# Optimization experiments

Measured on AMD Instinct MI355X. Metric: run time of the kernel, lower is better.

Reference implementation:

```python
import jax, jax.numpy as jnp
import numpy as np

S, B = 16384, 1
E = 2048          # encoder_hidden_size * num_enc_direction
H = 1024          # decoder_hidden_size
L = 2             # num_layer_dec
C = 5             # num_classes


def setup_inputs() -> dict:
    key = jax.random.key(0)
    ks = jax.random.split(key, 16)
    s = lambda fan_in: 1.0 / np.sqrt(fan_in)
    inp = {
        "encoder_hiddens": jax.random.normal(ks[0], (S, B, E), jnp.float32),
        "hidden": jax.random.normal(ks[1], (L, B, H), jnp.float32),
        "c": jax.random.normal(ks[2], (L, B, H), jnp.float32),
        # attn_alpha: Linear(2H + E, 1)
        "attn_w": jax.random.uniform(ks[3], (1, 2 * H + E), jnp.float32, -s(2 * H + E), s(2 * H + E)),
        "attn_b": jax.random.uniform(ks[4], (1,), jnp.float32, -s(2 * H + E), s(2 * H + E)),
        # LSTM layer 0: input E -> H
        "w_ih_l0": jax.random.uniform(ks[5], (4 * H, E), jnp.float32, -s(H), s(H)),
        "w_hh_l0": jax.random.uniform(ks[6], (4 * H, H), jnp.float32, -s(H), s(H)),
        "b_ih_l0": jax.random.uniform(ks[7], (4 * H,), jnp.float32, -s(H), s(H)),
        "b_hh_l0": jax.random.uniform(ks[8], (4 * H,), jnp.float32, -s(H), s(H)),
        # LSTM layer 1: input H -> H
        "w_ih_l1": jax.random.uniform(ks[9], (4 * H, H), jnp.float32, -s(H), s(H)),
        "w_hh_l1": jax.random.uniform(ks[10], (4 * H, H), jnp.float32, -s(H), s(H)),
        "b_ih_l1": jax.random.uniform(ks[11], (4 * H,), jnp.float32, -s(H), s(H)),
        "b_hh_l1": jax.random.uniform(ks[12], (4 * H,), jnp.float32, -s(H), s(H)),
        # fc: Linear(H, C)
        "fc_w": jax.random.uniform(ks[13], (C, H), jnp.float32, -s(H), s(H)),
        "fc_b": jax.random.uniform(ks[14], (C,), jnp.float32, -s(H), s(H)),
    }
    return inp


def _lstm_cell(x, h, c, w_ih, w_hh, b_ih, b_hh):
    # PyTorch gate order: i, f, g, o
    gates = x @ w_ih.T + b_ih + h @ w_hh.T + b_hh  # [B, 4H]
    i, f, g, o = jnp.split(gates, 4, axis=-1)
    c2 = jax.nn.sigmoid(f) * c + jax.nn.sigmoid(i) * jnp.tanh(g)
    h2 = jax.nn.sigmoid(o) * jnp.tanh(c2)
    return h2, c2


def reference(encoder_hiddens, hidden, c, attn_w, attn_b,
              w_ih_l0, w_hh_l0, b_ih_l0, b_hh_l0,
              w_ih_l1, w_hh_l1, b_ih_l1, b_hh_l1,
              fc_w, fc_b):
    h0, c0 = hidden[0], c[0]  # [B, H]
    # Vectorized per-timestep attn_alpha(concat(h0, c0, enc_i)):
    # split attn_w columns over [h0 | c0 | enc] and fuse the static part.
    w_h, w_c, w_e = attn_w[:, :H], attn_w[:, H:2 * H], attn_w[:, 2 * H:]
    static = h0 @ w_h.T + c0 @ w_c.T + attn_b            # [B, 1]
    scores = jnp.einsum('sbe,oe->sbo', encoder_hiddens, w_e) + static  # [S, B, 1]
    # Original applies softmax over dim=1 of a [B=1, 1] tensor per step -> all ones.
    attn = jax.nn.softmax(scores, axis=-1)               # [S, B, 1], identically 1.0
    # bmm(enc[B,E,S], attn[B,S,1]) == weighted sum over S
    attn_applied = jnp.einsum('sbe,sb->be', encoder_hiddens, attn[..., 0])  # [B, E]

    # 2-layer LSTM, single timestep
    h1, c1 = _lstm_cell(attn_applied, hidden[0], c[0], w_ih_l0, w_hh_l0, b_ih_l0, b_hh_l0)
    h2, c2 = _lstm_cell(h1, hidden[1], c[1], w_ih_l1, w_hh_l1, b_ih_l1, b_hh_l1)

    out = h2  # [B, H] == out.view(1*B, H)
    return out @ fc_w.T + fc_b  # [B, C]
```

## Files before the change

### kernel.cpp

```cpp
#include <hip/hip_runtime.h>
#include <hip/hip_bf16.h>
#include <math.h>

#define S_LEN 16384
#define E_DIM 2048
#define H_DIM 1024
#define G_DIM 4096
#define C_DIM 5

#define RCH 256
#define ROWS_PER_CHUNK (S_LEN / RCH)

#define WS_PART   0
#define WS_COLSUM (WS_PART + RCH * E_DIM)
#define WS_H1     (WS_COLSUM + E_DIM)
#define WS_H2     (WS_H1 + H_DIM)

__global__ __launch_bounds__(256) void colsum_partial_k(
    const float4* __restrict__ enc, float4* __restrict__ part) {
  const int E4 = E_DIM / 4;
  int colgroup = blockIdx.x & 1;
  int chunk = blockIdx.x >> 1;
  int e4 = colgroup * 256 + threadIdx.x;
  float4 acc = {0.f, 0.f, 0.f, 0.f};
  int r0 = chunk * ROWS_PER_CHUNK;
#pragma unroll 8
  for (int r = r0; r < r0 + ROWS_PER_CHUNK; ++r) {
    float4 v = enc[(size_t)r * E4 + e4];
    acc.x += v.x; acc.y += v.y; acc.z += v.z; acc.w += v.w;
  }
  part[chunk * E4 + e4] = acc;
}

__global__ __launch_bounds__(256) void colsum_final_k(
    const float* __restrict__ part, float* __restrict__ colsum) {
  int e = blockIdx.x * blockDim.x + threadIdx.x;
  float acc = 0.f;
#pragma unroll 8
  for (int ch = 0; ch < RCH; ++ch) acc += part[(size_t)ch * E_DIM + e];
  colsum[e] = acc;
}

__global__ __launch_bounds__(256) void lstm_fused_k(
    const float4* __restrict__ w_ih, const float4* __restrict__ w_hh,
    const float* __restrict__ b_ih, const float* __restrict__ b_hh,
    const float4* __restrict__ x, int xlen4,
    const float4* __restrict__ h, int hlen4,
    const float* __restrict__ c_prev,
    float* __restrict__ h_out) {
  __shared__ float smem[4];
  int wave = threadIdx.x >> 6;
  int lane = threadIdx.x & 63;
  int j = blockIdx.x;
  int row = wave * H_DIM + j;

  float acc = 0.f;
  const float4* wi = w_ih + (size_t)row * xlen4;
#pragma unroll
  for (int k = lane; k < xlen4; k += 64) {
    float4 w4 = wi[k];
    float4 v = x[k];
    acc += w4.x * v.x + w4.y * v.y + w4.z * v.z + w4.w * v.w;
  }
  const float4* wh = w_hh + (size_t)row * hlen4;
#pragma unroll
  for (int k = lane; k < hlen4; k += 64) {
    float4 w4 = wh[k];
    float4 v = h[k];
    acc += w4.x * v.x + w4.y * v.y + w4.z * v.z + w4.w * v.w;
  }
#pragma unroll
  for (int off = 32; off > 0; off >>= 1) acc += __shfl_down(acc, off);
  if (lane == 0) smem[wave] = acc + b_ih[row] + b_hh[row];
  __syncthreads();
  if (threadIdx.x == 0) {
    float ig = smem[0], fg = smem[1], gg = smem[2], og = smem[3];
    float si = 1.f / (1.f + expf(-ig));
    float sf = 1.f / (1.f + expf(-fg));
    float so = 1.f / (1.f + expf(-og));
    float c2 = sf * c_prev[j] + si * tanhf(gg);
    h_out[j] = so * tanhf(c2);
  }
}

__global__ __launch_bounds__(320) void fc_k(
    const float4* __restrict__ fc_w, const float* __restrict__ fc_b,
    const float4* __restrict__ h2, float* __restrict__ out) {
  int wave = threadIdx.x >> 6;
  int lane = threadIdx.x & 63;
  if (wave >= C_DIM) return;
  const int H4 = H_DIM / 4;
  float acc = 0.f;
  const float4* wr = fc_w + (size_t)wave * H4;
#pragma unroll
  for (int k = lane; k < H4; k += 64) {
    float4 w4 = wr[k];
    float4 v = h2[k];
    acc += w4.x * v.x + w4.y * v.y + w4.z * v.z + w4.w * v.w;
  }
#pragma unroll
  for (int off = 32; off > 0; off >>= 1) acc += __shfl_down(acc, off);
  if (lane == 0) out[wave] = acc + fc_b[wave];
}

extern "C" void kernel_launch(void* const* d_in, const int* in_sizes, int n_in,
                              void* d_out, int out_size, void* d_ws, size_t ws_size,
                              hipStream_t stream) {
  const float* enc     = (const float*)d_in[0];
  const float* hidden  = (const float*)d_in[1];
  const float* c_in    = (const float*)d_in[2];
  const float* w_ih_l0 = (const float*)d_in[5];
  const float* w_hh_l0 = (const float*)d_in[6];
  const float* b_ih_l0 = (const float*)d_in[7];
  const float* b_hh_l0 = (const float*)d_in[8];
  const float* w_ih_l1 = (const float*)d_in[9];
  const float* w_hh_l1 = (const float*)d_in[10];
  const float* b_ih_l1 = (const float*)d_in[11];
  const float* b_hh_l1 = (const float*)d_in[12];
  const float* fc_w    = (const float*)d_in[13];
  const float* fc_b    = (const float*)d_in[14];

  float* ws = (float*)d_ws;
  float* part   = ws + WS_PART;
  float* colsum = ws + WS_COLSUM;
  float* h1     = ws + WS_H1;
  float* h2     = ws + WS_H2;
  float* out    = (float*)d_out;

  colsum_partial_k<<<2 * RCH, 256, 0, stream>>>((const float4*)enc, (float4*)part);
  colsum_final_k<<<E_DIM / 256, 256, 0, stream>>>(part, colsum);

  lstm_fused_k<<<H_DIM, 256, 0, stream>>>(
      (const float4*)w_ih_l0, (const float4*)w_hh_l0, b_ih_l0, b_hh_l0,
      (const float4*)colsum, E_DIM / 4, (const float4*)hidden, H_DIM / 4,
      c_in, h1);

  lstm_fused_k<<<H_DIM, 256, 0, stream>>>(
      (const float4*)w_ih_l1, (const float4*)w_hh_l1, b_ih_l1, b_hh_l1,
      (const float4*)h1, H_DIM / 4, (const float4*)(hidden + H_DIM), H_DIM / 4,
      c_in + H_DIM, h2);

  fc_k<<<1, 320, 0, stream>>>((const float4*)fc_w, fc_b, (const float4*)h2, out);
}
```

Measured before the change: 62.03 us.

## Fuse decoder pipeline into one persistent kernel with grid-wide barriers

Replaces the five separate launches (two column-sum stages, two LSTM layers, fc) with a single 512-block kernel that moves between stages through atomic-counter grid barriers, after a memset that clears the barrier counters. The column sum now reduces rows within each block in shared memory first, so only 64 partial rows go to memory instead of 256. Each LSTM block now handles two hidden units, reusing the loaded x/h vectors across two weight rows. This aims to remove launch gaps and inter-kernel idle time, but relies on all 512 blocks being co-resident and adds spin-wait barrier overhead.

```diff
diff --git a/kernel.cpp b/kernel.cpp
--- a/kernel.cpp
+++ b/kernel.cpp
@@ -5,76 +5,91 @@
 #define S_LEN 16384
 #define E_DIM 2048
 #define H_DIM 1024
-#define G_DIM 4096
 #define C_DIM 5
 
-#define RCH 256
-#define ROWS_PER_CHUNK (S_LEN / RCH)
-
-#define WS_PART   0
-#define WS_COLSUM (WS_PART + RCH * E_DIM)
-#define WS_H1     (WS_COLSUM + E_DIM)
-#define WS_H2     (WS_H1 + H_DIM)
-
-__global__ __launch_bounds__(256) void colsum_partial_k(
-    const float4* __restrict__ enc, float4* __restrict__ part) {
-  const int E4 = E_DIM / 4;
-  int colgroup = blockIdx.x & 1;
-  int chunk = blockIdx.x >> 1;
-  int e4 = colgroup * 256 + threadIdx.x;
-  float4 acc = {0.f, 0.f, 0.f, 0.f};
-  int r0 = chunk * ROWS_PER_CHUNK;
-#pragma unroll 8
-  for (int r = r0; r < r0 + ROWS_PER_CHUNK; ++r) {
-    float4 v = enc[(size_t)r * E4 + e4];
-    acc.x += v.x; acc.y += v.y; acc.z += v.z; acc.w += v.w;
-  }
-  part[chunk * E4 + e4] = acc;
-}
-
-__global__ __launch_bounds__(256) void colsum_final_k(
-    const float* __restrict__ part, float* __restrict__ colsum) {
-  int e = blockIdx.x * blockDim.x + threadIdx.x;
-  float acc = 0.f;
-#pragma unroll 8
-  for (int ch = 0; ch < RCH; ++ch) acc += part[(size_t)ch * E_DIM + e];
-  colsum[e] = acc;
-}
-
-__global__ __launch_bounds__(256) void lstm_fused_k(
-    const float4* __restrict__ w_ih, const float4* __restrict__ w_hh,
-    const float* __restrict__ b_ih, const float* __restrict__ b_hh,
-    const float4* __restrict__ x, int xlen4,
-    const float4* __restrict__ h, int hlen4,
-    const float* __restrict__ c_prev,
-    float* __restrict__ h_out) {
-  __shared__ float smem[4];
-  int wave = threadIdx.x >> 6;
-  int lane = threadIdx.x & 63;
-  int j = blockIdx.x;
-  int row = wave * H_DIM + j;
-
-  float acc = 0.f;
-  const float4* wi = w_ih + (size_t)row * xlen4;
-#pragma unroll
-  for (int k = lane; k < xlen4; k += 64) {
-    float4 w4 = wi[k];
-    float4 v = x[k];
-    acc += w4.x * v.x + w4.y * v.y + w4.z * v.z + w4.w * v.w;
-  }
-  const float4* wh = w_hh + (size_t)row * hlen4;
-#pragma unroll
-  for (int k = lane; k < hlen4; k += 64) {
-    float4 w4 = wh[k];
-    float4 v = h[k];
-    acc += w4.x * v.x + w4.y * v.y + w4.z * v.z + w4.w * v.w;
-  }
-#pragma unroll
-  for (int off = 32; off > 0; off >>= 1) acc += __shfl_down(acc, off);
-  if (lane == 0) smem[wave] = acc + b_ih[row] + b_hh[row];
+#define NB 512
+#define NT 256
+
+#define NCTR 16
+#define BAR_BYTES (4 * NCTR * 16 * 4)
+
+__device__ __forceinline__ void gbar(int* bars, int k) {
   __syncthreads();
   if (threadIdx.x == 0) {
-    float ig = smem[0], fg = smem[1], gg = smem[2], og = smem[3];
+    __threadfence();
+    int* ctr = bars + (k * NCTR + (blockIdx.x & (NCTR - 1))) * 16;
+    __hip_atomic_fetch_add(ctr, 1, __ATOMIC_RELEASE, __HIP_MEMORY_SCOPE_AGENT);
+    int done = 0;
+    while (!done) {
+      int s = 0;
+#pragma unroll
+      for (int i = 0; i < NCTR; ++i)
+        s += __hip_atomic_load(bars + (k * NCTR + i) * 16, __ATOMIC_RELAXED,
+                               __HIP_MEMORY_SCOPE_AGENT);
+      done = (s == NB);
+      if (!done) __builtin_amdgcn_s_sleep(8);
+    }
+    __threadfence();
+  }
+  __syncthreads();
+}
+
+__device__ __forceinline__ float wave_sum(float v) {
+#pragma unroll
+  for (int off = 32; off > 0; off >>= 1) v += __shfl_down(v, off);
+  return v;
+}
+
+__device__ __forceinline__ float dot4(float4 a, float4 b) {
+  return a.x * b.x + a.y * b.y + a.z * b.z + a.w * b.w;
+}
+
+__device__ __forceinline__ void lstm_layer(
+    const float4* __restrict__ w_ih, int xlen4,
+    const float4* __restrict__ w_hh,
+    const float* __restrict__ b_ih, const float* __restrict__ b_hh,
+    const float4* __restrict__ x, const float4* __restrict__ h,
+    const float* __restrict__ c_prev, float* __restrict__ h_out,
+    float* smemf) {
+  int w = threadIdx.x >> 6;
+  int lane = threadIdx.x & 63;
+  int j0 = blockIdx.x * 2;
+  int rowA = w * H_DIM + j0;
+
+  float aA = 0.f, aB = 0.f;
+  const float4* wiA = w_ih + (size_t)rowA * xlen4;
+  const float4* wiB = wiA + xlen4;
+#pragma unroll 4
+  for (int k = lane; k < xlen4; k += 64) {
+    float4 xv = x[k];
+    float4 wa = wiA[k];
+    float4 wb = wiB[k];
+    aA += dot4(wa, xv);
+    aB += dot4(wb, xv);
+  }
+  const float4* whA = w_hh + (size_t)rowA * 256;
+  const float4* whB = whA + 256;
+#pragma unroll 4
+  for (int k = lane; k < 256; k += 64) {
+    float4 hv = h[k];
+    float4 wa = whA[k];
+    float4 wb = whB[k];
+    aA += dot4(wa, hv);
+    aB += dot4(wb, hv);
+  }
+  aA = wave_sum(aA);
+  aB = wave_sum(aB);
+  if (lane == 0) {
+    smemf[w * 2 + 0] = aA + b_ih[rowA] + b_hh[rowA];
+    smemf[w * 2 + 1] = aB + b_ih[rowA + 1] + b_hh[rowA + 1];
+  }
+  __syncthreads();
+  if (threadIdx.x < 2) {
+    int j = j0 + threadIdx.x;
+    float ig = smemf[0 + threadIdx.x];
+    float fg = smemf[2 + threadIdx.x];
+    float gg = smemf[4 + threadIdx.x];
+    float og = smemf[6 + threadIdx.x];
     float si = 1.f / (1.f + expf(-ig));
     float sf = 1.f / (1.f + expf(-fg));
     float so = 1.f / (1.f + expf(-og));
@@ -83,24 +98,83 @@
   }
 }
 
-__global__ __launch_bounds__(320) void fc_k(
-    const float4* __restrict__ fc_w, const float* __restrict__ fc_b,
-    const float4* __restrict__ h2, float* __restrict__ out) {
-  int wave = threadIdx.x >> 6;
-  int lane = threadIdx.x & 63;
-  if (wave >= C_DIM) return;
-  const int H4 = H_DIM / 4;
-  float acc = 0.f;
-  const float4* wr = fc_w + (size_t)wave * H4;
-#pragma unroll
-  for (int k = lane; k < H4; k += 64) {
-    float4 w4 = wr[k];
-    float4 v = h2[k];
-    acc += w4.x * v.x + w4.y * v.y + w4.z * v.z + w4.w * v.w;
-  }
-#pragma unroll
-  for (int off = 32; off > 0; off >>= 1) acc += __shfl_down(acc, off);
-  if (lane == 0) out[wave] = acc + fc_b[wave];
+__global__ __launch_bounds__(NT, 2) void decoder_mega_k(
+    const float* __restrict__ enc,
+    const float* __restrict__ hidden, const float* __restrict__ c_in,
+    const float* __restrict__ w_ih_l0, const float* __restrict__ w_hh_l0,
+    const float* __restrict__ b_ih_l0, const float* __restrict__ b_hh_l0,
+    const float* __restrict__ w_ih_l1, const float* __restrict__ w_hh_l1,
+    const float* __restrict__ b_ih_l1, const float* __restrict__ b_hh_l1,
+    const float* __restrict__ fc_w, const float* __restrict__ fc_b,
+    int* __restrict__ bars, float* __restrict__ part,
+    float* __restrict__ colsum, float* __restrict__ h1,
+    float* __restrict__ h2, float* __restrict__ out) {
+  __shared__ float4 smem4[NT];
+  float* smemf = (float*)smem4;
+
+  {
+    const float4* enc4 = (const float4*)enc;
+    int g = blockIdx.x >> 3;
+    int cb = blockIdx.x & 7;
+    int sub = threadIdx.x >> 6;
+    int lane = threadIdx.x & 63;
+    int c4 = cb * 64 + lane;
+    size_t base = ((size_t)(g * 256 + sub * 64)) * 512 + c4;
+    float4 acc = {0.f, 0.f, 0.f, 0.f};
+#pragma unroll 8
+    for (int r = 0; r < 64; ++r) {
+      float4 v = enc4[base + (size_t)r * 512];
+      acc.x += v.x; acc.y += v.y; acc.z += v.z; acc.w += v.w;
+    }
+    smem4[threadIdx.x] = acc;
+    __syncthreads();
+    if (threadIdx.x < 64) {
+      float4 a = smem4[threadIdx.x];
+      float4 b = smem4[64 + threadIdx.x];
+      float4 c = smem4[128 + threadIdx.x];
+      float4 d = smem4[192 + threadIdx.x];
+      float4 s;
+      s.x = (a.x + b.x) + (c.x + d.x);
+      s.y = (a.y + b.y) + (c.y + d.y);
+      s.z = (a.z + b.z) + (c.z + d.z);
+      s.w = (a.w + b.w) + (c.w + d.w);
+      ((float4*)part)[(size_t)g * 512 + cb * 64 + threadIdx.x] = s;
+    }
+  }
+  gbar(bars, 0);
+
+  if (blockIdx.x < 8) {
+    int col = blockIdx.x * NT + threadIdx.x;
+    float s = 0.f;
+#pragma unroll 8
+    for (int g = 0; g < 64; ++g) s += part[(size_t)g * E_DIM + col];
+    colsum[col] = s;
+  }
+  gbar(bars, 1);
+
+  lstm_layer((const float4*)w_ih_l0, E_DIM / 4, (const float4*)w_hh_l0,
+             b_ih_l0, b_hh_l0, (const float4*)colsum, (const float4*)hidden,
+             c_in, h1, smemf);
+  gbar(bars, 2);
+
+  lstm_layer((const float4*)w_ih_l1, H_DIM / 4, (const float4*)w_hh_l1,
+             b_ih_l1, b_hh_l1, (const float4*)h1,
+             (const float4*)(hidden + H_DIM), c_in + H_DIM, h2, smemf);
+  gbar(bars, 3);
+
+  if (blockIdx.x == 0) {
+    int w = threadIdx.x >> 6;
+    int lane = threadIdx.x & 63;
+    const float4* h24 = (const float4*)h2;
+    for (int r = w; r < C_DIM; r += 4) {
+      const float4* wr4 = (const float4*)fc_w + (size_t)r * 256;
+      float a = 0.f;
+#pragma unroll 4
+      for (int k = lane; k < 256; k += 64) a += dot4(wr4[k], h24[k]);
+      a = wave_sum(a);
+      if (lane == 0) out[r] = a + fc_b[r];
+    }
+  }
 }
 
 extern "C" void kernel_launch(void* const* d_in, const int* in_sizes, int n_in,
@@ -120,25 +194,18 @@
   const float* fc_w    = (const float*)d_in[13];
   const float* fc_b    = (const float*)d_in[14];
 
-  float* ws = (float*)d_ws;
-  float* part   = ws + WS_PART;
-  float* colsum = ws + WS_COLSUM;
-  float* h1     = ws + WS_H1;
-  float* h2     = ws + WS_H2;
+  int* bars = (int*)d_ws;
+  float* fws = (float*)((char*)d_ws + 4096);
+  float* part   = fws;
+  float* colsum = part + 64 * E_DIM;
+  float* h1     = colsum + E_DIM;
+  float* h2     = h1 + H_DIM;
   float* out    = (float*)d_out;
 
-  colsum_partial_k<<<2 * RCH, 256, 0, stream>>>((const float4*)enc, (float4*)part);
-  colsum_final_k<<<E_DIM / 256, 256, 0, stream>>>(part, colsum);
-
-  lstm_fused_k<<<H_DIM, 256, 0, stream>>>(
-      (const float4*)w_ih_l0, (const float4*)w_hh_l0, b_ih_l0, b_hh_l0,
-      (const float4*)colsum, E_DIM / 4, (const float4*)hidden, H_DIM / 4,
-      c_in, h1);
-
-  lstm_fused_k<<<H_DIM, 256, 0, stream>>>(
-      (const float4*)w_ih_l1, (const float4*)w_hh_l1, b_ih_l1, b_hh_l1,
-      (const float4*)h1, H_DIM / 4, (const float4*)(hidden + H_DIM), H_DIM / 4,
-      c_in + H_DIM, h2);
-
-  fc_k<<<1, 320, 0, stream>>>((const float4*)fc_w, fc_b, (const float4*)h2, out);
-}
+  hipMemsetAsync(d_ws, 0, BAR_BYTES, stream);
+
+  decoder_mega_k<<<NB, NT, 0, stream>>>(
+      enc, hidden, c_in, w_ih_l0, w_hh_l0, b_ih_l0, b_hh_l0,
+      w_ih_l1, w_hh_l1, b_ih_l1, b_hh_l1, fc_w, fc_b,
+      bars, part, colsum, h1, h2, out);
+}
```

After: 192.2 us. 210% more time.

## Restructure LSTM gate GEMVs to contiguous rows and fuse cell updates downstream

Applied to the files above, without the earlier changes.

The per-hidden-unit LSTM kernel is split into a gate-GEMV kernel whose blocks cover four consecutive gate rows, instead of one row from each gate block. The cell nonlinearity is moved into the next kernel: layer-0 cell math is recomputed redundantly by every block of the layer-1 gate kernel into shared memory, and layer-1 cell math is fused into the FC kernel. The column-sum reduction is split into twice as many chunks, and its final pass now has four waves share each column. The redundant per-block cell recomputation (1024 elements, four transcendentals each) adds compute to every block, and a single block now does all of the layer-1 cell math.

```diff
diff --git a/kernel.cpp b/kernel.cpp
--- a/kernel.cpp
+++ b/kernel.cpp
@@ -8,13 +8,25 @@
 #define G_DIM 4096
 #define C_DIM 5
 
-#define RCH 256
-#define ROWS_PER_CHUNK (S_LEN / RCH)
+#define CS_CHUNKS 512
+#define CS_ROWS   (S_LEN / CS_CHUNKS)
 
 #define WS_PART   0
-#define WS_COLSUM (WS_PART + RCH * E_DIM)
-#define WS_H1     (WS_COLSUM + E_DIM)
-#define WS_H2     (WS_H1 + H_DIM)
+#define WS_COLSUM (WS_PART + CS_CHUNKS * E_DIM)
+#define WS_G0     (WS_COLSUM + E_DIM)
+#define WS_G1     (WS_G0 + G_DIM)
+
+__device__ __forceinline__ float wave_sum(float v) {
+#pragma unroll
+  for (int off = 32; off > 0; off >>= 1) v += __shfl_down(v, off);
+  return v;
+}
+
+__device__ __forceinline__ float dot4(float4 a, float4 b) {
+  return a.x * b.x + a.y * b.y + a.z * b.z + a.w * b.w;
+}
+
+__device__ __forceinline__ float sigm(float x) { return 1.f / (1.f + expf(-x)); }
 
 __global__ __launch_bounds__(256) void colsum_partial_k(
     const float4* __restrict__ enc, float4* __restrict__ part) {
@@ -23,84 +35,113 @@
   int chunk = blockIdx.x >> 1;
   int e4 = colgroup * 256 + threadIdx.x;
   float4 acc = {0.f, 0.f, 0.f, 0.f};
-  int r0 = chunk * ROWS_PER_CHUNK;
+  size_t base = (size_t)chunk * CS_ROWS * E4 + e4;
 #pragma unroll 8
-  for (int r = r0; r < r0 + ROWS_PER_CHUNK; ++r) {
-    float4 v = enc[(size_t)r * E4 + e4];
+  for (int r = 0; r < CS_ROWS; ++r) {
+    float4 v = enc[base + (size_t)r * E4];
     acc.x += v.x; acc.y += v.y; acc.z += v.z; acc.w += v.w;
   }
-  part[chunk * E4 + e4] = acc;
+  part[(size_t)chunk * E4 + e4] = acc;
 }
 
 __global__ __launch_bounds__(256) void colsum_final_k(
     const float* __restrict__ part, float* __restrict__ colsum) {
-  int e = blockIdx.x * blockDim.x + threadIdx.x;
+  __shared__ float red[4][64];
+  int lane = threadIdx.x & 63;
+  int grp = threadIdx.x >> 6;
+  int col = blockIdx.x * 64 + lane;
   float acc = 0.f;
+  int c0 = grp * (CS_CHUNKS / 4);
 #pragma unroll 8
-  for (int ch = 0; ch < RCH; ++ch) acc += part[(size_t)ch * E_DIM + e];
-  colsum[e] = acc;
-}
-
-__global__ __launch_bounds__(256) void lstm_fused_k(
-    const float4* __restrict__ w_ih, const float4* __restrict__ w_hh,
-    const float* __restrict__ b_ih, const float* __restrict__ b_hh,
-    const float4* __restrict__ x, int xlen4,
-    const float4* __restrict__ h, int hlen4,
-    const float* __restrict__ c_prev,
-    float* __restrict__ h_out) {
-  __shared__ float smem[4];
-  int wave = threadIdx.x >> 6;
-  int lane = threadIdx.x & 63;
-  int j = blockIdx.x;
-  int row = wave * H_DIM + j;
-
-  float acc = 0.f;
-  const float4* wi = w_ih + (size_t)row * xlen4;
-#pragma unroll
-  for (int k = lane; k < xlen4; k += 64) {
-    float4 w4 = wi[k];
-    float4 v = x[k];
-    acc += w4.x * v.x + w4.y * v.y + w4.z * v.z + w4.w * v.w;
-  }
-  const float4* wh = w_hh + (size_t)row * hlen4;
-#pragma unroll
-  for (int k = lane; k < hlen4; k += 64) {
-    float4 w4 = wh[k];
-    float4 v = h[k];
-    acc += w4.x * v.x + w4.y * v.y + w4.z * v.z + w4.w * v.w;
-  }
-#pragma unroll
-  for (int off = 32; off > 0; off >>= 1) acc += __shfl_down(acc, off);
-  if (lane == 0) smem[wave] = acc + b_ih[row] + b_hh[row];
+  for (int ch = c0; ch < c0 + CS_CHUNKS / 4; ++ch)
+    acc += part[(size_t)ch * E_DIM + col];
+  red[grp][lane] = acc;
   __syncthreads();
-  if (threadIdx.x == 0) {
-    float ig = smem[0], fg = smem[1], gg = smem[2], og = smem[3];
-    float si = 1.f / (1.f + expf(-ig));
-    float sf = 1.f / (1.f + expf(-fg));
-    float so = 1.f / (1.f + expf(-og));
-    float c2 = sf * c_prev[j] + si * tanhf(gg);
-    h_out[j] = so * tanhf(c2);
+  if (threadIdx.x < 64) {
+    float s = (red[0][lane] + red[1][lane]) + (red[2][lane] + red[3][lane]);
+    colsum[col] = s;
   }
 }
 
-__global__ __launch_bounds__(320) void fc_k(
-    const float4* __restrict__ fc_w, const float* __restrict__ fc_b,
-    const float4* __restrict__ h2, float* __restrict__ out) {
+__global__ __launch_bounds__(256) void gates0_k(
+    const float4* __restrict__ w_ih, const float4* __restrict__ w_hh,
+    const float* __restrict__ b_ih, const float* __restrict__ b_hh,
+    const float4* __restrict__ x, const float4* __restrict__ h,
+    float* __restrict__ gates) {
   int wave = threadIdx.x >> 6;
   int lane = threadIdx.x & 63;
-  if (wave >= C_DIM) return;
-  const int H4 = H_DIM / 4;
+  int row = blockIdx.x * 4 + wave;
+
   float acc = 0.f;
-  const float4* wr = fc_w + (size_t)wave * H4;
+  const float4* wi = w_ih + (size_t)row * 512;
 #pragma unroll
-  for (int k = lane; k < H4; k += 64) {
-    float4 w4 = wr[k];
-    float4 v = h2[k];
-    acc += w4.x * v.x + w4.y * v.y + w4.z * v.z + w4.w * v.w;
+  for (int k = lane; k < 512; k += 64) acc += dot4(wi[k], x[k]);
+  const float4* wh = w_hh + (size_t)row * 256;
+#pragma unroll
+  for (int k = lane; k < 256; k += 64) acc += dot4(wh[k], h[k]);
+  acc = wave_sum(acc);
+  if (lane == 0) gates[row] = acc + b_ih[row] + b_hh[row];
+}
+
+__global__ __launch_bounds__(256) void gates1_cell0_k(
+    const float* __restrict__ g0, const float* __restrict__ c0,
+    const float4* __restrict__ w_ih, const float4* __restrict__ w_hh,
+    const float* __restrict__ b_ih, const float* __restrict__ b_hh,
+    const float4* __restrict__ h,
+    float* __restrict__ gates) {
+  __shared__ __align__(16) float h1s[H_DIM];
+#pragma unroll
+  for (int k = 0; k < 4; ++k) {
+    int j = threadIdx.x + 256 * k;
+    float ig = g0[j], fg = g0[H_DIM + j], gg = g0[2 * H_DIM + j],
+          og = g0[3 * H_DIM + j];
+    float c2 = sigm(fg) * c0[j] + sigm(ig) * tanhf(gg);
+    h1s[j] = sigm(og) * tanhf(c2);
   }
+  __syncthreads();
+
+  int wave = threadIdx.x >> 6;
+  int lane = threadIdx.x & 63;
+  int row = blockIdx.x * 4 + wave;
+  const float4* h1s4 = (const float4*)h1s;
+
+  float acc = 0.f;
+  const float4* wi = w_ih + (size_t)row * 256;
 #pragma unroll
-  for (int off = 32; off > 0; off >>= 1) acc += __shfl_down(acc, off);
-  if (lane == 0) out[wave] = acc + fc_b[wave];
+  for (int k = lane; k < 256; k += 64) acc += dot4(wi[k], h1s4[k]);
+  const float4* wh = w_hh + (size_t)row * 256;
+#pragma unroll
+  for (int k = lane; k < 256; k += 64) acc += dot4(wh[k], h[k]);
+  acc = wave_sum(acc);
+  if (lane == 0) gates[row] = acc + b_ih[row] + b_hh[row];
+}
+
+__global__ __launch_bounds__(512) void fc_cell1_k(
+    const float* __restrict__ g1, const float* __restrict__ c1,
+    const float4* __restrict__ fc_w, const float* __restrict__ fc_b,
+    float* __restrict__ out) {
+  __shared__ __align__(16) float h2s[H_DIM];
+#pragma unroll
+  for (int k = 0; k < 2; ++k) {
+    int j = threadIdx.x + 512 * k;
+    float ig = g1[j], fg = g1[H_DIM + j], gg = g1[2 * H_DIM + j],
+          og = g1[3 * H_DIM + j];
+    float c2 = sigm(fg) * c1[j] + sigm(ig) * tanhf(gg);
+    h2s[j] = sigm(og) * tanhf(c2);
+  }
+  __syncthreads();
+
+  int wave = threadIdx.x >> 6;
+  int lane = threadIdx.x & 63;
+  if (wave < C_DIM) {
+    const float4* h24 = (const float4*)h2s;
+    const float4* wr = fc_w + (size_t)wave * 256;
+    float acc = 0.f;
+#pragma unroll
+    for (int k = lane; k < 256; k += 64) acc += dot4(wr[k], h24[k]);
+    acc = wave_sum(acc);
+    if (lane == 0) out[wave] = acc + fc_b[wave];
+  }
 }
 
 extern "C" void kernel_launch(void* const* d_in, const int* in_sizes, int n_in,
@@ -123,22 +164,23 @@
   float* ws = (float*)d_ws;
   float* part   = ws + WS_PART;
   float* colsum = ws + WS_COLSUM;
-  float* h1     = ws + WS_H1;
-  float* h2     = ws + WS_H2;
+  float* g0     = ws + WS_G0;
+  float* g1     = ws + WS_G1;
   float* out    = (float*)d_out;
 
-  colsum_partial_k<<<2 * RCH, 256, 0, stream>>>((const float4*)enc, (float4*)part);
-  colsum_final_k<<<E_DIM / 256, 256, 0, stream>>>(part, colsum);
+  colsum_partial_k<<<2 * CS_CHUNKS, 256, 0, stream>>>(
+      (const float4*)enc, (float4*)part);
+  colsum_final_k<<<E_DIM / 64, 256, 0, stream>>>(part, colsum);
 
-  lstm_fused_k<<<H_DIM, 256, 0, stream>>>(
+  gates0_k<<<G_DIM / 4, 256, 0, stream>>>(
       (const float4*)w_ih_l0, (const float4*)w_hh_l0, b_ih_l0, b_hh_l0,
-      (const float4*)colsum, E_DIM / 4, (const float4*)hidden, H_DIM / 4,
-      c_in, h1);
+      (const float4*)colsum, (const float4*)hidden, g0);
 
-  lstm_fused_k<<<H_DIM, 256, 0, stream>>>(
+  gates1_cell0_k<<<G_DIM / 4, 256, 0, stream>>>(
+      g0, c_in,
       (const float4*)w_ih_l1, (const float4*)w_hh_l1, b_ih_l1, b_hh_l1,
-      (const float4*)h1, H_DIM / 4, (const float4*)(hidden + H_DIM), H_DIM / 4,
-      c_in + H_DIM, h2);
+      (const float4*)(hidden + H_DIM), g1);
 
-  fc_k<<<1, 320, 0, stream>>>((const float4*)fc_w, fc_b, (const float4*)h2, out);
+  fc_cell1_k<<<1, 512, 0, stream>>>(
+      g1, c_in + H_DIM, (const float4*)fc_w, fc_b, out);
 }
```

Result: faster. 55.40 us (-10.7%).

## Fuse decoder pipeline into one persistent kernel with atomic-counter grid barriers

Applied to the files above, without the earlier changes.

Replaces the five separate launches (two colsum passes, two LSTM layers, fc) with a single persistent kernel of 512 blocks that synchronize through global atomic counters and spin-waits. The W_hh·h0 product for layer 0 is computed before waiting for the encoder column sum, so it overlaps the reduction. The last 16 blocks to arrive finish the column sum. The LSTM gate nonlinearities are recomputed redundantly in every block from shared gate buffers. This removes launch gaps and intermediate kernel boundaries. It relies on all 512 blocks being co-resident and adds a memset launch plus spin overhead.

```diff
diff --git a/kernel.cpp b/kernel.cpp
--- a/kernel.cpp
+++ b/kernel.cpp
@@ -8,99 +8,193 @@
 #define G_DIM 4096
 #define C_DIM 5
 
-#define RCH 256
-#define ROWS_PER_CHUNK (S_LEN / RCH)
-
-#define WS_PART   0
-#define WS_COLSUM (WS_PART + RCH * E_DIM)
-#define WS_H1     (WS_COLSUM + E_DIM)
-#define WS_H2     (WS_H1 + H_DIM)
-
-__global__ __launch_bounds__(256) void colsum_partial_k(
-    const float4* __restrict__ enc, float4* __restrict__ part) {
-  const int E4 = E_DIM / 4;
-  int colgroup = blockIdx.x & 1;
-  int chunk = blockIdx.x >> 1;
-  int e4 = colgroup * 256 + threadIdx.x;
-  float4 acc = {0.f, 0.f, 0.f, 0.f};
-  int r0 = chunk * ROWS_PER_CHUNK;
+#define NB 512
+#define NT 512
+#define ROWS_PER_BLK (S_LEN / NB)
+#define NFIN 16
+#define FIN_COLS (E_DIM / NFIN)
+
+#define CTR_BYTES 1024
+
+__device__ __forceinline__ float dload(const float* p) {
+  return __hip_atomic_load((float*)p, __ATOMIC_RELAXED, __HIP_MEMORY_SCOPE_AGENT);
+}
+__device__ __forceinline__ void dstore(float* p, float v) {
+  __hip_atomic_store(p, v, __ATOMIC_RELAXED, __HIP_MEMORY_SCOPE_AGENT);
+}
+__device__ __forceinline__ int aload(int* p) {
+  return __hip_atomic_load(p, __ATOMIC_RELAXED, __HIP_MEMORY_SCOPE_AGENT);
+}
+__device__ __forceinline__ void spin_until(int* ctr, int target) {
+  for (int it = 0; it < (1 << 22); ++it) {
+    if (aload(ctr) >= target) return;
+    __builtin_amdgcn_s_sleep(2);
+  }
+}
+
+__device__ __forceinline__ float wave_sum(float v) {
+#pragma unroll
+  for (int off = 32; off > 0; off >>= 1) v += __shfl_down(v, off);
+  return v;
+}
+__device__ __forceinline__ float dot4(float4 a, float4 b) {
+  return a.x * b.x + a.y * b.y + a.z * b.z + a.w * b.w;
+}
+__device__ __forceinline__ float sigm(float x) { return 1.f / (1.f + expf(-x)); }
+
+__global__ __launch_bounds__(NT, 4) void decoder_persist_k(
+    const float* __restrict__ enc,
+    const float* __restrict__ hidden, const float* __restrict__ c_in,
+    const float* __restrict__ w_ih_l0, const float* __restrict__ w_hh_l0,
+    const float* __restrict__ b_ih_l0, const float* __restrict__ b_hh_l0,
+    const float* __restrict__ w_ih_l1, const float* __restrict__ w_hh_l1,
+    const float* __restrict__ b_ih_l1, const float* __restrict__ b_hh_l1,
+    const float* __restrict__ fc_w, const float* __restrict__ fc_b,
+    int* __restrict__ ctr, float* __restrict__ partial,
+    float* __restrict__ colsum, float* __restrict__ g0,
+    float* __restrict__ g1, float* __restrict__ out) {
+  __shared__ __align__(16) float xs[E_DIM];
+  __shared__ __align__(16) float h1s[H_DIM];
+  __shared__ float red2[NT];
+  __shared__ int tk;
+
+  const int tid = threadIdx.x;
+  const int b = blockIdx.x;
+  const int wave = tid >> 6;
+  const int lane = tid & 63;
+  const int row = b * 8 + wave;
+
+  {
+    const float4* enc4 = (const float4*)enc;
+    float4 acc = {0.f, 0.f, 0.f, 0.f};
+    size_t base = (size_t)b * ROWS_PER_BLK * (E_DIM / 4) + tid;
 #pragma unroll 8
-  for (int r = r0; r < r0 + ROWS_PER_CHUNK; ++r) {
-    float4 v = enc[(size_t)r * E4 + e4];
-    acc.x += v.x; acc.y += v.y; acc.z += v.z; acc.w += v.w;
-  }
-  part[chunk * E4 + e4] = acc;
-}
-
-__global__ __launch_bounds__(256) void colsum_final_k(
-    const float* __restrict__ part, float* __restrict__ colsum) {
-  int e = blockIdx.x * blockDim.x + threadIdx.x;
-  float acc = 0.f;
+    for (int r = 0; r < ROWS_PER_BLK; ++r) {
+      float4 v = enc4[base + (size_t)r * (E_DIM / 4)];
+      acc.x += v.x; acc.y += v.y; acc.z += v.z; acc.w += v.w;
+    }
+    ((float4*)xs)[tid] = acc;
+    __syncthreads();
+#pragma unroll 4
+    for (int i = 0; i < 4; ++i)
+      dstore(&partial[(size_t)b * E_DIM + i * NT + tid], xs[i * NT + tid]);
+  }
+  asm volatile("s_waitcnt vmcnt(0)" ::: "memory");
+  __syncthreads();
+  if (tid == 0)
+    tk = __hip_atomic_fetch_add(&ctr[0], 1, __ATOMIC_RELAXED,
+                                __HIP_MEMORY_SCOPE_AGENT);
+  __syncthreads();
+  const int ticket = tk;
+
+  float hh = 0.f;
+  {
+    const float4* h0g = (const float4*)hidden;
+    const float4* wh = (const float4*)w_hh_l0 + (size_t)row * 256;
+#pragma unroll
+    for (int k = lane; k < 256; k += 64) hh += dot4(wh[k], h0g[k]);
+  }
+
+  if (ticket >= NB - NFIN) {
+    int f = ticket - (NB - NFIN);
+    if (tid == 0) spin_until(&ctr[0], NB);
+    __syncthreads();
+    int col = f * FIN_COLS + (tid & 127);
+    int grp = tid >> 7;
+    float a = 0.f;
 #pragma unroll 8
-  for (int ch = 0; ch < RCH; ++ch) acc += part[(size_t)ch * E_DIM + e];
-  colsum[e] = acc;
-}
-
-__global__ __launch_bounds__(256) void lstm_fused_k(
-    const float4* __restrict__ w_ih, const float4* __restrict__ w_hh,
-    const float* __restrict__ b_ih, const float* __restrict__ b_hh,
-    const float4* __restrict__ x, int xlen4,
-    const float4* __restrict__ h, int hlen4,
-    const float* __restrict__ c_prev,
-    float* __restrict__ h_out) {
-  __shared__ float smem[4];
-  int wave = threadIdx.x >> 6;
-  int lane = threadIdx.x & 63;
-  int j = blockIdx.x;
-  int row = wave * H_DIM + j;
-
-  float acc = 0.f;
-  const float4* wi = w_ih + (size_t)row * xlen4;
-#pragma unroll
-  for (int k = lane; k < xlen4; k += 64) {
-    float4 w4 = wi[k];
-    float4 v = x[k];
-    acc += w4.x * v.x + w4.y * v.y + w4.z * v.z + w4.w * v.w;
-  }
-  const float4* wh = w_hh + (size_t)row * hlen4;
-#pragma unroll
-  for (int k = lane; k < hlen4; k += 64) {
-    float4 w4 = wh[k];
-    float4 v = h[k];
-    acc += w4.x * v.x + w4.y * v.y + w4.z * v.z + w4.w * v.w;
-  }
-#pragma unroll
-  for (int off = 32; off > 0; off >>= 1) acc += __shfl_down(acc, off);
-  if (lane == 0) smem[wave] = acc + b_ih[row] + b_hh[row];
-  __syncthreads();
-  if (threadIdx.x == 0) {
-    float ig = smem[0], fg = smem[1], gg = smem[2], og = smem[3];
-    float si = 1.f / (1.f + expf(-ig));
-    float sf = 1.f / (1.f + expf(-fg));
-    float so = 1.f / (1.f + expf(-og));
-    float c2 = sf * c_prev[j] + si * tanhf(gg);
-    h_out[j] = so * tanhf(c2);
-  }
-}
-
-__global__ __launch_bounds__(320) void fc_k(
-    const float4* __restrict__ fc_w, const float* __restrict__ fc_b,
-    const float4* __restrict__ h2, float* __restrict__ out) {
-  int wave = threadIdx.x >> 6;
-  int lane = threadIdx.x & 63;
-  if (wave >= C_DIM) return;
-  const int H4 = H_DIM / 4;
-  float acc = 0.f;
-  const float4* wr = fc_w + (size_t)wave * H4;
-#pragma unroll
-  for (int k = lane; k < H4; k += 64) {
-    float4 w4 = wr[k];
-    float4 v = h2[k];
-    acc += w4.x * v.x + w4.y * v.y + w4.z * v.z + w4.w * v.w;
-  }
-#pragma unroll
-  for (int off = 32; off > 0; off >>= 1) acc += __shfl_down(acc, off);
-  if (lane == 0) out[wave] = acc + fc_b[wave];
+    for (int c = grp * 128; c < grp * 128 + 128; ++c)
+      a += dload(&partial[(size_t)c * E_DIM + col]);
+    red2[grp * 128 + (tid & 127)] = a;
+    __syncthreads();
+    if (tid < 128) {
+      float s = (red2[tid] + red2[128 + tid]) + (red2[256 + tid] + red2[384 + tid]);
+      dstore(&colsum[f * FIN_COLS + tid], s);
+    }
+    asm volatile("s_waitcnt vmcnt(0)" ::: "memory");
+    __syncthreads();
+    if (tid == 0)
+      (void)__hip_atomic_fetch_add(&ctr[16], 1, __ATOMIC_RELAXED,
+                                   __HIP_MEMORY_SCOPE_AGENT);
+  }
+
+  if (tid == 0) spin_until(&ctr[16], NFIN);
+  __syncthreads();
+#pragma unroll 4
+  for (int i = 0; i < 4; ++i) xs[i * NT + tid] = dload(&colsum[i * NT + tid]);
+  __syncthreads();
+  {
+    float ih = 0.f;
+    const float4* wi = (const float4*)w_ih_l0 + (size_t)row * 512;
+    const float4* xs4 = (const float4*)xs;
+#pragma unroll
+    for (int k = lane; k < 512; k += 64) ih += dot4(wi[k], xs4[k]);
+    float tot = wave_sum(ih + hh);
+    if (lane == 0) dstore(&g0[row], tot + b_ih_l0[row] + b_hh_l0[row]);
+  }
+  asm volatile("s_waitcnt vmcnt(0)" ::: "memory");
+  __syncthreads();
+  if (tid == 0)
+    (void)__hip_atomic_fetch_add(&ctr[32], 1, __ATOMIC_RELAXED,
+                                 __HIP_MEMORY_SCOPE_AGENT);
+
+  if (tid == 0) spin_until(&ctr[32], NB);
+  __syncthreads();
+#pragma unroll
+  for (int u = 0; u < 2; ++u) {
+    int j = tid + u * NT;
+    float ig = dload(&g0[j]);
+    float fg = dload(&g0[H_DIM + j]);
+    float gg = dload(&g0[2 * H_DIM + j]);
+    float og = dload(&g0[3 * H_DIM + j]);
+    float c2 = sigm(fg) * c_in[j] + sigm(ig) * tanhf(gg);
+    h1s[j] = sigm(og) * tanhf(c2);
+  }
+  __syncthreads();
+
+  {
+    const float4* h1g = (const float4*)(hidden + H_DIM);
+    const float4* h14 = (const float4*)h1s;
+    const float4* wi = (const float4*)w_ih_l1 + (size_t)row * 256;
+    const float4* wh = (const float4*)w_hh_l1 + (size_t)row * 256;
+    float a = 0.f;
+#pragma unroll
+    for (int k = lane; k < 256; k += 64) a += dot4(wi[k], h14[k]) + dot4(wh[k], h1g[k]);
+    float tot = wave_sum(a);
+    if (lane == 0) dstore(&g1[row], tot + b_ih_l1[row] + b_hh_l1[row]);
+  }
+  asm volatile("s_waitcnt vmcnt(0)" ::: "memory");
+  __syncthreads();
+  if (tid == 0)
+    (void)__hip_atomic_fetch_add(&ctr[48], 1, __ATOMIC_RELAXED,
+                                 __HIP_MEMORY_SCOPE_AGENT);
+
+  if (b < C_DIM) {
+    if (tid == 0) spin_until(&ctr[48], NB);
+    __syncthreads();
+    const float* c1 = c_in + H_DIM;
+#pragma unroll
+    for (int u = 0; u < 2; ++u) {
+      int j = tid + u * NT;
+      float ig = dload(&g1[j]);
+      float fg = dload(&g1[H_DIM + j]);
+      float gg = dload(&g1[2 * H_DIM + j]);
+      float og = dload(&g1[3 * H_DIM + j]);
+      float c2 = sigm(fg) * c1[j] + sigm(ig) * tanhf(gg);
+      h1s[j] = sigm(og) * tanhf(c2);
+    }
+    __syncthreads();
+    float p = fc_w[(size_t)b * H_DIM + tid] * h1s[tid] +
+              fc_w[(size_t)b * H_DIM + NT + tid] * h1s[NT + tid];
+    red2[tid] = p;
+    __syncthreads();
+#pragma unroll
+    for (int s = NT / 2; s > 0; s >>= 1) {
+      if (tid < s) red2[tid] += red2[tid + s];
+      __syncthreads();
+    }
+    if (tid == 0) out[b] = red2[0] + fc_b[b];
+  }
 }
 
 extern "C" void kernel_launch(void* const* d_in, const int* in_sizes, int n_in,
@@ -120,25 +214,17 @@
   const float* fc_w    = (const float*)d_in[13];
   const float* fc_b    = (const float*)d_in[14];
 
-  float* ws = (float*)d_ws;
-  float* part   = ws + WS_PART;
-  float* colsum = ws + WS_COLSUM;
-  float* h1     = ws + WS_H1;
-  float* h2     = ws + WS_H2;
-  float* out    = (float*)d_out;
-
-  colsum_partial_k<<<2 * RCH, 256, 0, stream>>>((const float4*)enc, (float4*)part);
-  colsum_final_k<<<E_DIM / 256, 256, 0, stream>>>(part, colsum);
-
-  lstm_fused_k<<<H_DIM, 256, 0, stream>>>(
-      (const float4*)w_ih_l0, (const float4*)w_hh_l0, b_ih_l0, b_hh_l0,
-      (const float4*)colsum, E_DIM / 4, (const float4*)hidden, H_DIM / 4,
-      c_in, h1);
-
-  lstm_fused_k<<<H_DIM, 256, 0, stream>>>(
-      (const float4*)w_ih_l1, (const float4*)w_hh_l1, b_ih_l1, b_hh_l1,
-      (const float4*)h1, H_DIM / 4, (const float4*)(hidden + H_DIM), H_DIM / 4,
-      c_in + H_DIM, h2);
-
-  fc_k<<<1, 320, 0, stream>>>((const float4*)fc_w, fc_b, (const float4*)h2, out);
-}
+  int* ctr = (int*)d_ws;
+  float* partial = (float*)((char*)d_ws + CTR_BYTES);
+  float* colsum  = partial + (size_t)NB * E_DIM;
+  float* g0      = colsum + E_DIM;
+  float* g1      = g0 + G_DIM;
+  float* out     = (float*)d_out;
+
+  hipMemsetAsync(d_ws, 0, CTR_BYTES, stream);
+
+  decoder_persist_k<<<NB, NT, 0, stream>>>(
+      enc, hidden, c_in, w_ih_l0, w_hh_l0, b_ih_l0, b_hh_l0,
+      w_ih_l1, w_hh_l1, b_ih_l1, b_hh_l1, fc_w, fc_b,
+      ctr, partial, colsum, g0, g1, out);
+}
```

Result: slower. 93.24 us (+50.3%).
